# Kernel optimization log

Measured on AMD Instinct MI355X. Metric: run time of the kernel, lower is better.

The kernel has to match this reference:

```python
import jax, jax.numpy as jnp
import numpy as np

B, S, C, H = 2, 3144, 256, 8
HD = C // H                      # head_dim = key_dim = 32
SCALE = HD ** -0.5
QN = 8                           # queriesNum hard-coded in source
KS = 5                           # lepe depthwise conv kernel


def setup_inputs() -> dict:
    key = jax.random.key(0)
    ks = jax.random.split(key, 10)
    gain_qkv = 2 ** (-2.5) * (2.0 / (C + C)) ** 0.5  # xavier_normal std with gain 2^-2.5
    gain_out = (2.0 / (C + C)) ** 0.5
    return {
        "x": jax.random.normal(ks[0], (B, S, C), jnp.float32),
        "mask": jax.random.uniform(ks[1], (B, S, S), jnp.float32),
        "wq": jax.random.normal(ks[2], (C, C), jnp.float32) * gain_qkv,
        "bq": jnp.zeros((C,), jnp.float32),
        "wk": jax.random.normal(ks[3], (C, C), jnp.float32) * gain_qkv,
        "bk": jnp.zeros((C,), jnp.float32),
        "wv": jax.random.normal(ks[4], (C, C), jnp.float32) * gain_qkv,
        "bv": jnp.zeros((C,), jnp.float32),
        "lepe_w": jax.random.normal(ks[5], (KS, KS, 1, C), jnp.float32) * 0.05,  # depthwise HWIO
        "lepe_b": jnp.zeros((C,), jnp.float32),
        "wo": jax.random.normal(ks[6], (C, C), jnp.float32) * gain_out,
        "bo": jnp.zeros((C,), jnp.float32),
        "h": 56,
        "w": 56,
    }


def _dwconv(x_nhwc, kern, bias):
    # depthwise 5x5, stride 1, padding 2 (groups = channels)
    y = jax.lax.conv_general_dilated(
        x_nhwc, kern, window_strides=(1, 1), padding=((2, 2), (2, 2)),
        dimension_numbers=("NHWC", "HWIO", "NHWC"),
        feature_group_count=x_nhwc.shape[-1])
    return y + bias


def reference(x, mask, wq, bq, wk, bk, wv, bv, lepe_w, lepe_b, wo, bo, h, w):
    b, s, c = x.shape
    q = x @ wq.T + bq
    k = (x @ wk.T + bk) * SCALE
    v = x @ wv.T + bv
    # lepe positional residual on the non-query tokens
    lepe = _dwconv(v[:, QN:].reshape(b, h, w, c), lepe_w, lepe_b).reshape(b, h * w, c)
    qh = q.reshape(b, s, H, HD).transpose(0, 2, 1, 3)   # (b, H, s, hd)
    kh = k.reshape(b, s, H, HD).transpose(0, 2, 1, 3)
    vh = kh  # faithful to source: v_h = k.reshape(...)  (scaled k used as values)
    qk = jnp.einsum("bhqd,bhkd->bhqk", qh, kh)
    qk = qk + jnp.log(mask[:, None] + 1e-6)              # isSoftMask=True path
    attn = jax.nn.softmax(qk, axis=-1)
    out = jnp.einsum("bhqk,bhkd->bhqd", attn, vh)
    out = out.transpose(0, 2, 1, 3).reshape(b, s, c)
    out = out.at[:, QN:].add(lepe)
    return out @ wo.T + bo
```

## Files before the change

kernel.cpp:

```cpp
#include <hip/hip_runtime.h>


#define S_LEN 3144
#define SP    3200
#define HEADS 8
#define HD    32
#define BATCH 2
#define MROWS (BATCH*S_LEN)
#define NPIX  3136
#define SCALE_F 0.17677669529663687f
#define KQ_SC   0.25504472665352026f

typedef __bf16 bf16x8  __attribute__((ext_vector_type(8)));
typedef __bf16 bf16x4  __attribute__((ext_vector_type(4)));
typedef float  floatx4 __attribute__((ext_vector_type(4)));
typedef short  shortx4 __attribute__((ext_vector_type(4)));

static __device__ __forceinline__ float bf2f(unsigned int h) {
  union { unsigned int u; float f; } v; v.u = h << 16; return v.f;
}
static __device__ __forceinline__ unsigned short f2bf(float f) {
  union { __bf16 b; unsigned short u; } v; v.b = (__bf16)f; return v.u;
}
static __device__ __forceinline__ bf16x8 ldcvt8(const float* __restrict__ p) {
  float4 a = *(const float4*)p;
  float4 b = *(const float4*)(p + 4);
  bf16x8 r;
  r[0]=(__bf16)a.x; r[1]=(__bf16)a.y; r[2]=(__bf16)a.z; r[3]=(__bf16)a.w;
  r[4]=(__bf16)b.x; r[5]=(__bf16)b.y; r[6]=(__bf16)b.z; r[7]=(__bf16)b.w;
  return r;
}

#define GLOBAL_AS __attribute__((address_space(1)))
#define LDS_AS    __attribute__((address_space(3)))
static __device__ __forceinline__ void gload_lds16(const void* g, void* l) {
  __builtin_amdgcn_global_load_lds((const GLOBAL_AS void*)g, (LDS_AS void*)l, 16, 0, 0);
}

#define FENCE4() asm volatile("s_waitcnt vmcnt(4)" ::: "memory")
#define FENCE0() asm volatile("s_waitcnt vmcnt(0)" ::: "memory")

__global__ __launch_bounds__(256) void k_cvt(
    const float* __restrict__ x, const float* __restrict__ wq,
    const float* __restrict__ wk, const float* __restrict__ wv,
    unsigned short* __restrict__ xb, unsigned short* __restrict__ w3b)
{
  const int i = blockIdx.x * 256 + threadIdx.x;
  const int NX = MROWS * 32;
  const int NW = 8192;
  const float* src;
  unsigned short* dst;
  if (i < NX) { src = x + (size_t)i * 8; dst = xb + (size_t)i * 8; }
  else {
    const int j = i - NX;
    if (j >= 3 * NW) return;
    src = (j < NW) ? wq + (size_t)j * 8
        : (j < 2 * NW) ? wk + (size_t)(j - NW) * 8
                       : wv + (size_t)(j - 2 * NW) * 8;
    dst = w3b + (size_t)j * 8;
  }
  bf16x8 v = ldcvt8(src);
  *(bf16x8*)dst = v;
}

__global__ __launch_bounds__(256) void k_qkv(
    const unsigned short* __restrict__ xb, const unsigned short* __restrict__ w3b,
    const float* __restrict__ bqp, const float* __restrict__ bkp,
    const float* __restrict__ bvp,
    unsigned short* __restrict__ qws, unsigned short* __restrict__ kws,
    unsigned short* __restrict__ vfrag, unsigned short* __restrict__ vstage)
{
  __shared__ unsigned short lds_t[64 * 65];
  const int lane = threadIdx.x & 63;
  const int wid  = threadIdx.x >> 6;
  const int c    = lane & 15, quad = lane >> 4;
  const int bsel  = blockIdx.x / 50;
  const int stile = blockIdx.x % 50;
  const int srow0 = stile * 64;
  const int ncol = blockIdx.y * 64;
  const int wsel = ncol >> 8;
  const int col0 = ncol & 255;

  const float* bptr = (wsel == 0) ? bqp : (wsel == 1) ? bkp : bvp;

  const int srow = srow0 + wid * 16 + c;
  const int arow = bsel * S_LEN + ((srow < S_LEN) ? srow : 0);
  const unsigned short* ap = xb  + (size_t)arow * 256 + quad * 8;
  const unsigned short* bp = w3b + (size_t)(ncol + c) * 256 + quad * 8;

  floatx4 acc[4];
#pragma unroll
  for (int ct = 0; ct < 4; ++ct) acc[ct] = (floatx4){0.f, 0.f, 0.f, 0.f};

#pragma unroll
  for (int ks = 0; ks < 8; ++ks) {
    bf16x8 af = *(const bf16x8*)(ap + ks * 32);
#pragma unroll
    for (int ct = 0; ct < 4; ++ct) {
      bf16x8 bf = *(const bf16x8*)(bp + (size_t)ct * 16 * 256 + ks * 32);
      acc[ct] = __builtin_amdgcn_mfma_f32_16x16x32_bf16(af, bf, acc[ct], 0, 0, 0);
    }
  }

#pragma unroll
  for (int ct = 0; ct < 4; ++ct) {
    const int col = col0 + ct * 16 + c;
    const float bias = bptr[col];
#pragma unroll
    for (int r = 0; r < 4; ++r) {
      const int s = srow0 + wid * 16 + quad * 4 + r;
      const int valid = (s < S_LEN);
      const float v = acc[ct][r] + bias;
      if (wsel == 0) {
        qws[(((size_t)(bsel * HEADS + (col >> 5))) * SP + s) * HD + (col & 31)] =
            valid ? f2bf(v) : (unsigned short)0;
      } else if (wsel == 1) {
        kws[(((size_t)(bsel * HEADS + (col >> 5))) * SP + s) * HD + (col & 31)] =
            valid ? f2bf(v * KQ_SC) : (unsigned short)0;
        lds_t[(ct * 16 + c) * 65 + (wid * 16 + quad * 4 + r)] =
            valid ? f2bf(v * SCALE_F) : (unsigned short)0;
      } else {
        if (valid) vstage[(size_t)(bsel * S_LEN + s) * 256 + col] = f2bf(v);
      }
    }
  }

  if (wsel == 1) {
    __syncthreads();
    const int tid = threadIdx.x;
#pragma unroll
    for (int j = 0; j < 4; ++j) {
      const int grp  = j * 4 + (tid >> 6);
      const int l    = tid & 63;
      const int ct2  = grp & 3;
      const int half = (grp >> 2) & 1;
      const int hsel = grp >> 3;
      const int cc = l & 15, qq = l >> 4;
      const int cl = hsel * 32 + half * 16 + cc;
      const int rb = ct2 * 16 + qq * 4;
      union { shortx4 s4; unsigned short u[4]; } pk;
#pragma unroll
      for (int e = 0; e < 4; ++e) pk.u[e] = lds_t[cl * 65 + rb + e];
      const int hglob = (col0 >> 5) + hsel;
      const size_t off =
          ((((size_t)(bsel * HEADS + hglob) * 50 + stile) * 4 + ct2) * 2 + half) * 64 + l;
      *(shortx4*)(vfrag + off * 4) = pk.s4;
    }
  }
}

__global__ __launch_bounds__(256) void k_lepe(const unsigned short* __restrict__ vws,
                                              const float* __restrict__ cw,
                                              const float* __restrict__ cb,
                                              unsigned short* __restrict__ lepe)
{
  int idx = blockIdx.x * 256 + threadIdx.x;
  if (idx >= BATCH * NPIX * 32) return;
  const int cg = idx & 31;
  const int p  = (idx >> 5) % NPIX;
  const int b  = idx / (NPIX * 32);
  const int y  = p / 56, xx = p - y * 56;

  float acc[8];
  {
    float4 b0 = *(const float4*)(cb + cg * 8);
    float4 b1 = *(const float4*)(cb + cg * 8 + 4);
    acc[0]=b0.x; acc[1]=b0.y; acc[2]=b0.z; acc[3]=b0.w;
    acc[4]=b1.x; acc[5]=b1.y; acc[6]=b1.z; acc[7]=b1.w;
  }
#pragma unroll
  for (int dy = -2; dy <= 2; ++dy) {
    const int yy = y + dy;
    if ((unsigned)yy >= 56u) continue;
#pragma unroll
    for (int dx = -2; dx <= 2; ++dx) {
      const int xs = xx + dx;
      if ((unsigned)xs >= 56u) continue;
      uint4 vv = *(const uint4*)(vws + (size_t)(b * S_LEN + 8 + yy * 56 + xs) * 256 + cg * 8);
      const float* wp = cw + (size_t)((dy + 2) * 5 + (dx + 2)) * 256 + cg * 8;
      float4 w0 = *(const float4*)wp;
      float4 w1 = *(const float4*)(wp + 4);
      unsigned int va[4] = {vv.x, vv.y, vv.z, vv.w};
      acc[0] += bf2f(va[0] & 0xFFFFu) * w0.x;  acc[1] += bf2f(va[0] >> 16) * w0.y;
      acc[2] += bf2f(va[1] & 0xFFFFu) * w0.z;  acc[3] += bf2f(va[1] >> 16) * w0.w;
      acc[4] += bf2f(va[2] & 0xFFFFu) * w1.x;  acc[5] += bf2f(va[2] >> 16) * w1.y;
      acc[6] += bf2f(va[3] & 0xFFFFu) * w1.z;  acc[7] += bf2f(va[3] >> 16) * w1.w;
    }
  }
  unsigned int o[4];
#pragma unroll
  for (int j = 0; j < 4; ++j)
    o[j] = (unsigned int)f2bf(acc[2*j]) | ((unsigned int)f2bf(acc[2*j+1]) << 16);
  *((uint4*)(lepe + (size_t)(b * NPIX + p) * 256 + cg * 8)) = make_uint4(o[0], o[1], o[2], o[3]);
}

template<bool TAIL>
static __device__ __forceinline__ void proc_tile(
    int t, const unsigned short* __restrict__ kb,
    const unsigned short* __restrict__ vb,
    const float* __restrict__ mb,
    int c, int quad, int lane, const bf16x8 qf,
    floatx4& o0, floatx4& o1, float& l_run)
{
  const int k0 = t * 64;
  bf16x8 kf[4]; shortx4 v0[4], v1[4];
  const unsigned short* tb = vb + (size_t)t * 2048;
#pragma unroll
  for (int ct = 0; ct < 4; ++ct) {
    kf[ct] = *(const bf16x8*)(kb + (size_t)(k0 + ct * 16 + c) * HD + quad * 8);
    v0[ct] = *(const shortx4*)(tb + (ct * 2 + 0) * 256 + lane * 4);
    v1[ct] = *(const shortx4*)(tb + (ct * 2 + 1) * 256 + lane * 4);
  }
  floatx4 s[4];
#pragma unroll
  for (int ct = 0; ct < 4; ++ct)
    s[ct] = __builtin_amdgcn_mfma_f32_16x16x32_bf16(kf[ct], qf,
               (floatx4){0.f,0.f,0.f,0.f}, 0, 0, 0);
  float ls = 0.f;
  shortx4 pf[4];
#pragma unroll
  for (int ct = 0; ct < 4; ++ct) {
    const float4 mv = *(const float4*)(mb + c * 64 + (((ct * 4 + quad) ^ c) * 4));
    float pr[4];
    pr[0] = (mv.x + 1e-6f) * __builtin_amdgcn_exp2f(s[ct][0]);
    pr[1] = (mv.y + 1e-6f) * __builtin_amdgcn_exp2f(s[ct][1]);
    pr[2] = (mv.z + 1e-6f) * __builtin_amdgcn_exp2f(s[ct][2]);
    pr[3] = (mv.w + 1e-6f) * __builtin_amdgcn_exp2f(s[ct][3]);
    if (TAIL) {
      const int kk = k0 + ct * 16 + quad * 4;
#pragma unroll
      for (int r = 0; r < 4; ++r) if (kk + r >= S_LEN) pr[r] = 0.f;
    }
    ls += (pr[0] + pr[1]) + (pr[2] + pr[3]);
    union { bf16x4 b4; shortx4 s4; } u;
    u.b4[0]=(__bf16)pr[0]; u.b4[1]=(__bf16)pr[1]; u.b4[2]=(__bf16)pr[2]; u.b4[3]=(__bf16)pr[3];
    pf[ct] = u.s4;
  }
  l_run += ls;
#pragma unroll
  for (int ct = 0; ct < 4; ++ct) {
    o0 = __builtin_amdgcn_mfma_f32_16x16x16bf16_1k(v0[ct], pf[ct], o0, 0, 0, 0);
    o1 = __builtin_amdgcn_mfma_f32_16x16x16bf16_1k(v1[ct], pf[ct], o1, 0, 0, 0);
  }
}

static __device__ __forceinline__ void stage_mask(
    const float* const (&msrc)[4], const int (&goff4)[4], int k0, float* dst)
{
#pragma unroll
  for (int i = 0; i < 4; ++i)
    gload_lds16(msrc[i] + (k0 + goff4[i]), dst + i * 256);
}

static __device__ __forceinline__ void stage_mask_tail(
    const float* const (&msrc)[4], const int (&goff4)[4], int k0, float* dst)
{
#pragma unroll
  for (int i = 0; i < 4; ++i) {
    int kk = k0 + goff4[i];
    if (kk > S_LEN - 4) kk = S_LEN - 4;
    gload_lds16(msrc[i] + kk, dst + i * 256);
  }
}

__global__ __launch_bounds__(512) void k_flash(
    const unsigned short* __restrict__ qws,
    const unsigned short* __restrict__ kws,
    const unsigned short* __restrict__ vfrag,
    const float* __restrict__ mask,
    const unsigned short* __restrict__ lepe,
    unsigned short* __restrict__ attn)
{
  __shared__ __align__(16) float smem[8][2048];
  const int lane = threadIdx.x & 63;
  const int wid  = threadIdx.x >> 6;
  const int c    = lane & 15, quad = lane >> 4;
  const int u    = blockIdx.x;
  const int xcd  = u & 7;
  const int slot = u >> 3;
  const int h    = slot & 7;
  const int p    = (slot >> 3) * 8 + xcd;
  const int b    = p / 200;
  const int strip = p - b * 200;
  const int qrow = strip * 16 + c;
  const size_t bh = (size_t)(b * HEADS + h);

  const bf16x8 qf = *(const bf16x8*)(qws + (bh * SP + qrow) * HD + quad * 8);
  const unsigned short* kb = kws + bh * SP * HD;
  const unsigned short* vb = vfrag + bh * (size_t)(50 * 2048);
  float* mt = &smem[wid][0];

  const float* msrc[4];
  int goff4[4];
#pragma unroll
  for (int i = 0; i < 4; ++i) {
    const int rq = i * 4 + (lane >> 4);
    int mr = strip * 16 + rq; if (mr >= S_LEN) mr = S_LEN - 1;
    msrc[i] = mask + ((size_t)b * S_LEN + mr) * S_LEN;
    goff4[i] = ((lane & 15) ^ rq) * 4;
  }

  float l_run = 0.f;
  floatx4 o0 = (floatx4){0.f,0.f,0.f,0.f};
  floatx4 o1 = (floatx4){0.f,0.f,0.f,0.f};

  const int tbase = wid * 6;
  const int nt = (wid < 2) ? 7 : 6;

  stage_mask(msrc, goff4, tbase * 64, mt);

  for (int it = 0; it < nt; ++it) {
    const int t = (it < 6) ? tbase + it : 48 + wid;
    if (it + 1 < nt) {
      const int tn = (it + 1 < 6) ? tbase + it + 1 : 48 + wid;
      float* dst = mt + ((it + 1) & 1) * 1024;
      if (tn == 49) stage_mask_tail(msrc, goff4, 49 * 64, dst);
      else          stage_mask(msrc, goff4, tn * 64, dst);
      FENCE4();
    } else {
      FENCE0();
    }
    const float* mb = mt + (it & 1) * 1024;
    if (wid == 1 && it == 6)
      proc_tile<true >(t, kb, vb, mb, c, quad, lane, qf, o0, o1, l_run);
    else
      proc_tile<false>(t, kb, vb, mb, c, quad, lane, qf, o0, o1, l_run);
  }

#pragma unroll
  for (int r = 0; r < 4; ++r) {
    smem[wid][lane * 9 + r]     = o0[r];
    smem[wid][lane * 9 + 4 + r] = o1[r];
  }
  smem[wid][lane * 9 + 8] = l_run;
  __syncthreads();

  if (wid == 0) {
#pragma unroll
    for (int w = 1; w < 8; ++w) {
#pragma unroll
      for (int r = 0; r < 4; ++r) {
        o0[r] += smem[w][lane * 9 + r];
        o1[r] += smem[w][lane * 9 + 4 + r];
      }
      l_run += smem[w][lane * 9 + 8];
    }
    l_run += __shfl_xor(l_run, 16);
    l_run += __shfl_xor(l_run, 32);
    const float rl = 1.f / l_run;

    if (qrow < S_LEN) {
      const size_t obase = ((size_t)b * S_LEN + qrow) * 256 + h * 32;
      const size_t lbase = (qrow >= 8) ? (((size_t)b * NPIX + (qrow - 8)) * 256 + h * 32) : 0;
#pragma unroll
      for (int mt2 = 0; mt2 < 2; ++mt2) {
        floatx4 ov = mt2 ? o1 : o0;
#pragma unroll
        for (int r = 0; r < 4; ++r) {
          const int d = mt2 * 16 + quad * 4 + r;
          float val = ov[r] * rl;
          if (qrow >= 8) val += bf2f(lepe[lbase + d]);
          attn[obase + d] = f2bf(val);
        }
      }
    }
  }
}

__global__ __launch_bounds__(256) void k_oproj(
    const unsigned short* __restrict__ attn,
    const float* __restrict__ wop,
    const float* __restrict__ bop,
    float* __restrict__ out)
{
  const int lane = threadIdx.x & 63;
  const int wid  = threadIdx.x >> 6;
  const int c = lane & 15, quad = lane >> 4;
  const int row0 = blockIdx.x * 64 + wid * 16;
  const int col0 = blockIdx.y * 64;

  int arow = row0 + c; if (arow >= MROWS) arow = 0;
  const unsigned short* ap = attn + (size_t)arow * 256 + quad * 8;
  const float* bp = wop + (size_t)(col0 + c) * 256 + quad * 8;

  floatx4 acc[4];
#pragma unroll
  for (int ct = 0; ct < 4; ++ct) acc[ct] = (floatx4){0.f,0.f,0.f,0.f};
#pragma unroll
  for (int ks = 0; ks < 8; ++ks) {
    bf16x8 af = *(const bf16x8*)(ap + ks * 32);
#pragma unroll
    for (int ct = 0; ct < 4; ++ct) {
      bf16x8 bf = ldcvt8(bp + (size_t)ct * 16 * 256 + ks * 32);
      acc[ct] = __builtin_amdgcn_mfma_f32_16x16x32_bf16(af, bf, acc[ct], 0, 0, 0);
    }
  }
#pragma unroll
  for (int ct = 0; ct < 4; ++ct) {
    const int col = col0 + ct * 16 + c;
    const float bias = bop[col];
#pragma unroll
    for (int r = 0; r < 4; ++r) {
      const int row = row0 + quad * 4 + r;
      if (row >= MROWS) continue;
      out[(size_t)row * 256 + col] = acc[ct][r] + bias;
    }
  }
}

#define QW_OFF 0u
#define KW_OFF 3276800u
#define VF_OFF 6553600u
#define LE_OFF 9830400u
#define AT_OFF 13041664u

extern "C" void kernel_launch(void* const* d_in, const int* in_sizes, int n_in,
                              void* d_out, int out_size, void* d_ws, size_t ws_size,
                              hipStream_t stream) {
  const float* x    = (const float*)d_in[0];
  const float* mask = (const float*)d_in[1];
  const float* wq   = (const float*)d_in[2];
  const float* bq   = (const float*)d_in[3];
  const float* wk   = (const float*)d_in[4];
  const float* bk   = (const float*)d_in[5];
  const float* wv   = (const float*)d_in[6];
  const float* bv   = (const float*)d_in[7];
  const float* lw   = (const float*)d_in[8];
  const float* lb   = (const float*)d_in[9];
  const float* wo   = (const float*)d_in[10];
  const float* bo   = (const float*)d_in[11];

  char* ws = (char*)d_ws;
  unsigned short* qws = (unsigned short*)(ws + QW_OFF);
  unsigned short* kws = (unsigned short*)(ws + KW_OFF);
  unsigned short* vfr = (unsigned short*)(ws + VF_OFF);
  unsigned short* w3b = (unsigned short*)(ws + LE_OFF);
  unsigned short* lpe = (unsigned short*)(ws + LE_OFF);
  unsigned short* atb = (unsigned short*)(ws + AT_OFF);
  unsigned short* vst = (unsigned short*)d_out;
  unsigned short* xb  = (unsigned short*)d_out + 1609728;
  float*          outf = (float*)d_out;

  k_cvt<<<882, 256, 0, stream>>>(x, wq, wk, wv, xb, w3b);
  k_qkv<<<dim3(100, 12), 256, 0, stream>>>(xb, w3b, bq, bk, bv, qws, kws, vfr, vst);
  k_lepe<<<784, 256, 0, stream>>>(vst, lw, lb, lpe);
  k_flash<<<3200, 512, 0, stream>>>(qws, kws, vfr, mask, lpe, atb);
  k_oproj<<<dim3(99, 4), 256, 0, stream>>>(atb, wo, bo, outf);
}
```

Before: 311.8 us.

## Prefetch K/V register fragments one tile ahead alongside mask staging

The attention loop is split into a load phase and a compute phase. K and V fragments for the next 64-key tile are now issued into a second register set at the same time as the async mask staging, and the loop is unrolled in pairs to alternate between the two buffers. The wait is raised to vmcnt(16) so the next tile's 16 loads can stay in flight while the current tile computes. This is meant to hide global-load latency on K/V, at the cost of more VGPRs, which could lower occupancy.

```diff
diff --git a/kernel.cpp b/kernel.cpp
--- a/kernel.cpp
+++ b/kernel.cpp
@@ -37,8 +37,8 @@
   __builtin_amdgcn_global_load_lds((const GLOBAL_AS void*)g, (LDS_AS void*)l, 16, 0, 0);
 }
 
-#define FENCE4() asm volatile("s_waitcnt vmcnt(4)" ::: "memory")
-#define FENCE0() asm volatile("s_waitcnt vmcnt(0)" ::: "memory")
+#define FENCE16() asm volatile("s_waitcnt vmcnt(16)" ::: "memory")
+#define FENCE0()  asm volatile("s_waitcnt vmcnt(0)" ::: "memory")
 
 __global__ __launch_bounds__(256) void k_cvt(
     const float* __restrict__ x, const float* __restrict__ wq,
@@ -194,16 +194,12 @@
   *((uint4*)(lepe + (size_t)(b * NPIX + p) * 256 + cg * 8)) = make_uint4(o[0], o[1], o[2], o[3]);
 }
 
-template<bool TAIL>
-static __device__ __forceinline__ void proc_tile(
-    int t, const unsigned short* __restrict__ kb,
-    const unsigned short* __restrict__ vb,
-    const float* __restrict__ mb,
-    int c, int quad, int lane, const bf16x8 qf,
-    floatx4& o0, floatx4& o1, float& l_run)
+static __device__ __forceinline__ void kv_load(
+    const unsigned short* __restrict__ kb, const unsigned short* __restrict__ vb,
+    int t, int c, int quad, int lane,
+    bf16x8 (&kf)[4], shortx4 (&v0)[4], shortx4 (&v1)[4])
 {
   const int k0 = t * 64;
-  bf16x8 kf[4]; shortx4 v0[4], v1[4];
   const unsigned short* tb = vb + (size_t)t * 2048;
 #pragma unroll
   for (int ct = 0; ct < 4; ++ct) {
@@ -211,6 +207,14 @@
     v0[ct] = *(const shortx4*)(tb + (ct * 2 + 0) * 256 + lane * 4);
     v1[ct] = *(const shortx4*)(tb + (ct * 2 + 1) * 256 + lane * 4);
   }
+}
+
+template<bool TAIL>
+static __device__ __forceinline__ void tile_compute(
+    int k0, const bf16x8 (&kf)[4], const shortx4 (&v0)[4], const shortx4 (&v1)[4],
+    const float* __restrict__ mb, int c, int quad, const bf16x8 qf,
+    floatx4& o0, floatx4& o1, float& l_run)
+{
   floatx4 s[4];
 #pragma unroll
   for (int ct = 0; ct < 4; ++ct)
@@ -305,26 +309,41 @@
   floatx4 o1 = (floatx4){0.f,0.f,0.f,0.f};
 
   const int tbase = wid * 6;
-  const int nt = (wid < 2) ? 7 : 6;
+  const bool hasExtra = (wid < 2);
+
+  bf16x8 kfA[4], kfB[4];
+  shortx4 v0A[4], v1A[4], v0B[4], v1B[4];
 
   stage_mask(msrc, goff4, tbase * 64, mt);
-
-  for (int it = 0; it < nt; ++it) {
-    const int t = (it < 6) ? tbase + it : 48 + wid;
-    if (it + 1 < nt) {
-      const int tn = (it + 1 < 6) ? tbase + it + 1 : 48 + wid;
-      float* dst = mt + ((it + 1) & 1) * 1024;
-      if (tn == 49) stage_mask_tail(msrc, goff4, 49 * 64, dst);
-      else          stage_mask(msrc, goff4, tn * 64, dst);
-      FENCE4();
+  kv_load(kb, vb, tbase, c, quad, lane, kfA, v0A, v1A);
+
+#pragma unroll 1
+  for (int jp = 0; jp < 3; ++jp) {
+    const int j0 = 2 * jp;
+    stage_mask(msrc, goff4, (tbase + j0 + 1) * 64, mt + 1024);
+    kv_load(kb, vb, tbase + j0 + 1, c, quad, lane, kfB, v0B, v1B);
+    FENCE16();
+    tile_compute<false>(0, kfA, v0A, v1A, mt, c, quad, qf, o0, o1, l_run);
+    if (jp < 2) {
+      stage_mask(msrc, goff4, (tbase + j0 + 2) * 64, mt);
+      kv_load(kb, vb, tbase + j0 + 2, c, quad, lane, kfA, v0A, v1A);
+      FENCE16();
+    } else if (hasExtra) {
+      if (wid == 0) stage_mask(msrc, goff4, 48 * 64, mt);
+      else          stage_mask_tail(msrc, goff4, 49 * 64, mt);
+      kv_load(kb, vb, 48 + wid, c, quad, lane, kfA, v0A, v1A);
+      FENCE16();
     } else {
       FENCE0();
     }
-    const float* mb = mt + (it & 1) * 1024;
-    if (wid == 1 && it == 6)
-      proc_tile<true >(t, kb, vb, mb, c, quad, lane, qf, o0, o1, l_run);
+    tile_compute<false>(0, kfB, v0B, v1B, mt + 1024, c, quad, qf, o0, o1, l_run);
+  }
+  if (hasExtra) {
+    FENCE0();
+    if (wid == 0)
+      tile_compute<false>(48 * 64, kfA, v0A, v1A, mt, c, quad, qf, o0, o1, l_run);
     else
-      proc_tile<false>(t, kb, vb, mb, c, quad, lane, qf, o0, o1, l_run);
+      tile_compute<true >(49 * 64, kfA, v0A, v1A, mt, c, quad, qf, o0, o1, l_run);
   }
 
 #pragma unroll
```

After: 345.9 us. +10.9%, slower.

## Put all eight heads in one flash block, split keys in halves, read mask directly

Applied to the files above, without the earlier changes.

The flash kernel now runs 400 blocks of 1024 threads. Each block covers one 16-row query strip for all 8 heads, and each head's key range is split across two waves. The old design staged the mask into LDS through global_load_lds double buffering. Now each lane reads its mask row straight from global memory, so the 8 head-waves sharing a strip can reuse the same mask rows through cache instead of fetching them 8 times across different blocks. The trade-offs are fewer, larger blocks (lower occupancy granularity), uncoalesced per-lane float4 mask reads, and longer serial loops per wave with no explicit prefetch.

```diff
diff --git a/kernel.cpp b/kernel.cpp
--- a/kernel.cpp
+++ b/kernel.cpp
@@ -30,15 +30,6 @@
   r[4]=(__bf16)b.x; r[5]=(__bf16)b.y; r[6]=(__bf16)b.z; r[7]=(__bf16)b.w;
   return r;
 }
-
-#define GLOBAL_AS __attribute__((address_space(1)))
-#define LDS_AS    __attribute__((address_space(3)))
-static __device__ __forceinline__ void gload_lds16(const void* g, void* l) {
-  __builtin_amdgcn_global_load_lds((const GLOBAL_AS void*)g, (LDS_AS void*)l, 16, 0, 0);
-}
-
-#define FENCE4() asm volatile("s_waitcnt vmcnt(4)" ::: "memory")
-#define FENCE0() asm volatile("s_waitcnt vmcnt(0)" ::: "memory")
 
 __global__ __launch_bounds__(256) void k_cvt(
     const float* __restrict__ x, const float* __restrict__ wq,
@@ -198,7 +189,7 @@
 static __device__ __forceinline__ void proc_tile(
     int t, const unsigned short* __restrict__ kb,
     const unsigned short* __restrict__ vb,
-    const float* __restrict__ mb,
+    const float* __restrict__ mp,
     int c, int quad, int lane, const bf16x8 qf,
     floatx4& o0, floatx4& o1, float& l_run)
 {
@@ -220,14 +211,16 @@
   shortx4 pf[4];
 #pragma unroll
   for (int ct = 0; ct < 4; ++ct) {
-    const float4 mv = *(const float4*)(mb + c * 64 + (((ct * 4 + quad) ^ c) * 4));
+    int kk = k0 + ct * 16 + quad * 4;
+    int kkl = kk;
+    if (TAIL) { if (kkl > S_LEN - 4) kkl = S_LEN - 4; }
+    const float4 mv = *(const float4*)(mp + kkl);
     float pr[4];
     pr[0] = (mv.x + 1e-6f) * __builtin_amdgcn_exp2f(s[ct][0]);
     pr[1] = (mv.y + 1e-6f) * __builtin_amdgcn_exp2f(s[ct][1]);
     pr[2] = (mv.z + 1e-6f) * __builtin_amdgcn_exp2f(s[ct][2]);
     pr[3] = (mv.w + 1e-6f) * __builtin_amdgcn_exp2f(s[ct][3]);
     if (TAIL) {
-      const int kk = k0 + ct * 16 + quad * 4;
 #pragma unroll
       for (int r = 0; r < 4; ++r) if (kk + r >= S_LEN) pr[r] = 0.f;
     }
@@ -244,26 +237,7 @@
   }
 }
 
-static __device__ __forceinline__ void stage_mask(
-    const float* const (&msrc)[4], const int (&goff4)[4], int k0, float* dst)
-{
-#pragma unroll
-  for (int i = 0; i < 4; ++i)
-    gload_lds16(msrc[i] + (k0 + goff4[i]), dst + i * 256);
-}
-
-static __device__ __forceinline__ void stage_mask_tail(
-    const float* const (&msrc)[4], const int (&goff4)[4], int k0, float* dst)
-{
-#pragma unroll
-  for (int i = 0; i < 4; ++i) {
-    int kk = k0 + goff4[i];
-    if (kk > S_LEN - 4) kk = S_LEN - 4;
-    gload_lds16(msrc[i] + kk, dst + i * 256);
-  }
-}
-
-__global__ __launch_bounds__(512) void k_flash(
+__global__ __launch_bounds__(1024) void k_flash(
     const unsigned short* __restrict__ qws,
     const unsigned short* __restrict__ kws,
     const unsigned short* __restrict__ vfrag,
@@ -271,80 +245,57 @@
     const unsigned short* __restrict__ lepe,
     unsigned short* __restrict__ attn)
 {
-  __shared__ __align__(16) float smem[8][2048];
+  __shared__ __align__(16) float red[8][64][9];
   const int lane = threadIdx.x & 63;
   const int wid  = threadIdx.x >> 6;
+  const int h    = wid & 7;
+  const int khalf = wid >> 3;
   const int c    = lane & 15, quad = lane >> 4;
+
   const int u    = blockIdx.x;
   const int xcd  = u & 7;
-  const int slot = u >> 3;
-  const int h    = slot & 7;
-  const int p    = (slot >> 3) * 8 + xcd;
-  const int b    = p / 200;
-  const int strip = p - b * 200;
+  const int j    = u >> 3;
+  const int b    = xcd & 1;
+  const int strip = j * 4 + (xcd >> 1);
   const int qrow = strip * 16 + c;
   const size_t bh = (size_t)(b * HEADS + h);
 
   const bf16x8 qf = *(const bf16x8*)(qws + (bh * SP + qrow) * HD + quad * 8);
   const unsigned short* kb = kws + bh * SP * HD;
   const unsigned short* vb = vfrag + bh * (size_t)(50 * 2048);
-  float* mt = &smem[wid][0];
-
-  const float* msrc[4];
-  int goff4[4];
-#pragma unroll
-  for (int i = 0; i < 4; ++i) {
-    const int rq = i * 4 + (lane >> 4);
-    int mr = strip * 16 + rq; if (mr >= S_LEN) mr = S_LEN - 1;
-    msrc[i] = mask + ((size_t)b * S_LEN + mr) * S_LEN;
-    goff4[i] = ((lane & 15) ^ rq) * 4;
-  }
+  const int mrow = (qrow < S_LEN) ? qrow : (S_LEN - 1);
+  const float* mp = mask + ((size_t)b * S_LEN + mrow) * S_LEN;
 
   float l_run = 0.f;
   floatx4 o0 = (floatx4){0.f,0.f,0.f,0.f};
   floatx4 o1 = (floatx4){0.f,0.f,0.f,0.f};
 
-  const int tbase = wid * 6;
-  const int nt = (wid < 2) ? 7 : 6;
-
-  stage_mask(msrc, goff4, tbase * 64, mt);
-
-  for (int it = 0; it < nt; ++it) {
-    const int t = (it < 6) ? tbase + it : 48 + wid;
-    if (it + 1 < nt) {
-      const int tn = (it + 1 < 6) ? tbase + it + 1 : 48 + wid;
-      float* dst = mt + ((it + 1) & 1) * 1024;
-      if (tn == 49) stage_mask_tail(msrc, goff4, 49 * 64, dst);
-      else          stage_mask(msrc, goff4, tn * 64, dst);
-      FENCE4();
-    } else {
-      FENCE0();
-    }
-    const float* mb = mt + (it & 1) * 1024;
-    if (wid == 1 && it == 6)
-      proc_tile<true >(t, kb, vb, mb, c, quad, lane, qf, o0, o1, l_run);
-    else
-      proc_tile<false>(t, kb, vb, mb, c, quad, lane, qf, o0, o1, l_run);
-  }
-
-#pragma unroll
-  for (int r = 0; r < 4; ++r) {
-    smem[wid][lane * 9 + r]     = o0[r];
-    smem[wid][lane * 9 + 4 + r] = o1[r];
-  }
-  smem[wid][lane * 9 + 8] = l_run;
+  const int t0 = khalf * 25;
+#pragma unroll 1
+  for (int jt = 0; jt < 24; ++jt)
+    proc_tile<false>(t0 + jt, kb, vb, mp, c, quad, lane, qf, o0, o1, l_run);
+  if (khalf == 0)
+    proc_tile<false>(24, kb, vb, mp, c, quad, lane, qf, o0, o1, l_run);
+  else
+    proc_tile<true >(49, kb, vb, mp, c, quad, lane, qf, o0, o1, l_run);
+
+  if (khalf) {
+#pragma unroll
+    for (int r = 0; r < 4; ++r) {
+      red[h][lane][r]     = o0[r];
+      red[h][lane][4 + r] = o1[r];
+    }
+    red[h][lane][8] = l_run;
+  }
   __syncthreads();
 
-  if (wid == 0) {
-#pragma unroll
-    for (int w = 1; w < 8; ++w) {
-#pragma unroll
-      for (int r = 0; r < 4; ++r) {
-        o0[r] += smem[w][lane * 9 + r];
-        o1[r] += smem[w][lane * 9 + 4 + r];
-      }
-      l_run += smem[w][lane * 9 + 8];
-    }
+  if (!khalf) {
+#pragma unroll
+    for (int r = 0; r < 4; ++r) {
+      o0[r] += red[h][lane][r];
+      o1[r] += red[h][lane][4 + r];
+    }
+    l_run += red[h][lane][8];
     l_run += __shfl_xor(l_run, 16);
     l_run += __shfl_xor(l_run, 32);
     const float rl = 1.f / l_run;
@@ -444,6 +395,6 @@
   k_cvt<<<882, 256, 0, stream>>>(x, wq, wk, wv, xb, w3b);
   k_qkv<<<dim3(100, 12), 256, 0, stream>>>(xb, w3b, bq, bk, bv, qws, kws, vfr, vst);
   k_lepe<<<784, 256, 0, stream>>>(vst, lw, lb, lpe);
-  k_flash<<<3200, 512, 0, stream>>>(qws, kws, vfr, mask, lpe, atb);
+  k_flash<<<400, 1024, 0, stream>>>(qws, kws, vfr, mask, lpe, atb);
   k_oproj<<<dim3(99, 4), 256, 0, stream>>>(atb, wo, bo, outf);
 }
```

New measurement: 337.7 us. +8.3%, slower.

## Precompute log2 mask into tiled swizzled layout before flash attention

Applied to the files above, without the earlier changes.

Adds a k_mprep kernel that converts the soft mask to log2(mask+1e-6) and writes it into a per-strip, per-tile swizzled buffer, with -1e30 in the padded tail columns. The flash kernel then streams this buffer contiguously and folds the mask into the exponent as exp2(s + logm), which removes the per-element multiply, the tail-masking branch and the clamped tail loads. The old path is kept as a fallback for when the workspace is too small for the roughly 82 MB buffer. The price is an extra full pass over the mask: one read plus one write of a slightly larger buffer. That traffic is likely to outweigh what the flash kernel saves.

```diff
diff --git a/kernel.cpp b/kernel.cpp
--- a/kernel.cpp
+++ b/kernel.cpp
@@ -61,6 +61,36 @@
   }
   bf16x8 v = ldcvt8(src);
   *(bf16x8*)dst = v;
+}
+
+__global__ __launch_bounds__(256) void k_mprep(const float* __restrict__ mask,
+                                               float* __restrict__ pm)
+{
+  const int bs = blockIdx.x;
+  const int b  = bs / 200, strip = bs % 200;
+  const int tid = threadIdx.x;
+  const int i  = tid >> 6, l = tid & 63;
+  const int rq = i * 4 + (l >> 4);
+  int mr = strip * 16 + rq; if (mr >= S_LEN) mr = S_LEN - 1;
+  const int cg = ((l & 15) ^ rq) & 15;
+  const float* src = mask + ((size_t)b * S_LEN + mr) * S_LEN;
+  float* dst = pm + (size_t)bs * (50 * 1024) + tid * 4;
+#pragma unroll 1
+  for (int tt = 0; tt < 10; ++tt) {
+    const int t = blockIdx.y * 10 + tt;
+    const int c0 = t * 64 + cg * 4;
+    float4 o;
+    if (c0 < S_LEN) {
+      float4 mv = *(const float4*)(src + c0);
+      o.x = __log2f(mv.x + 1e-6f);
+      o.y = __log2f(mv.y + 1e-6f);
+      o.z = __log2f(mv.z + 1e-6f);
+      o.w = __log2f(mv.w + 1e-6f);
+    } else {
+      o = make_float4(-1e30f, -1e30f, -1e30f, -1e30f);
+    }
+    *(float4*)(dst + (size_t)t * 1024) = o;
+  }
 }
 
 __global__ __launch_bounds__(256) void k_qkv(
@@ -194,8 +224,7 @@
   *((uint4*)(lepe + (size_t)(b * NPIX + p) * 256 + cg * 8)) = make_uint4(o[0], o[1], o[2], o[3]);
 }
 
-template<bool TAIL>
-static __device__ __forceinline__ void proc_tile(
+static __device__ __forceinline__ void proc_tile_pre(
     int t, const unsigned short* __restrict__ kb,
     const unsigned short* __restrict__ vb,
     const float* __restrict__ mb,
@@ -222,15 +251,10 @@
   for (int ct = 0; ct < 4; ++ct) {
     const float4 mv = *(const float4*)(mb + c * 64 + (((ct * 4 + quad) ^ c) * 4));
     float pr[4];
-    pr[0] = (mv.x + 1e-6f) * __builtin_amdgcn_exp2f(s[ct][0]);
-    pr[1] = (mv.y + 1e-6f) * __builtin_amdgcn_exp2f(s[ct][1]);
-    pr[2] = (mv.z + 1e-6f) * __builtin_amdgcn_exp2f(s[ct][2]);
-    pr[3] = (mv.w + 1e-6f) * __builtin_amdgcn_exp2f(s[ct][3]);
-    if (TAIL) {
-      const int kk = k0 + ct * 16 + quad * 4;
-#pragma unroll
-      for (int r = 0; r < 4; ++r) if (kk + r >= S_LEN) pr[r] = 0.f;
-    }
+    pr[0] = __builtin_amdgcn_exp2f(s[ct][0] + mv.x);
+    pr[1] = __builtin_amdgcn_exp2f(s[ct][1] + mv.y);
+    pr[2] = __builtin_amdgcn_exp2f(s[ct][2] + mv.z);
+    pr[3] = __builtin_amdgcn_exp2f(s[ct][3] + mv.w);
     ls += (pr[0] + pr[1]) + (pr[2] + pr[3]);
     union { bf16x4 b4; shortx4 s4; } u;
     u.b4[0]=(__bf16)pr[0]; u.b4[1]=(__bf16)pr[1]; u.b4[2]=(__bf16)pr[2]; u.b4[3]=(__bf16)pr[3];
@@ -244,30 +268,19 @@
   }
 }
 
-static __device__ __forceinline__ void stage_mask(
-    const float* const (&msrc)[4], const int (&goff4)[4], int k0, float* dst)
+static __device__ __forceinline__ void stage_pre(
+    const float* __restrict__ mp_t, int lane, float* dst)
 {
 #pragma unroll
   for (int i = 0; i < 4; ++i)
-    gload_lds16(msrc[i] + (k0 + goff4[i]), dst + i * 256);
-}
-
-static __device__ __forceinline__ void stage_mask_tail(
-    const float* const (&msrc)[4], const int (&goff4)[4], int k0, float* dst)
-{
-#pragma unroll
-  for (int i = 0; i < 4; ++i) {
-    int kk = k0 + goff4[i];
-    if (kk > S_LEN - 4) kk = S_LEN - 4;
-    gload_lds16(msrc[i] + kk, dst + i * 256);
-  }
-}
-
-__global__ __launch_bounds__(512) void k_flash(
+    gload_lds16(mp_t + i * 256 + lane * 4, dst + i * 256);
+}
+
+__global__ __launch_bounds__(512) void k_flash_pre(
     const unsigned short* __restrict__ qws,
     const unsigned short* __restrict__ kws,
     const unsigned short* __restrict__ vfrag,
-    const float* __restrict__ mask,
+    const float* __restrict__ pmask,
     const unsigned short* __restrict__ lepe,
     unsigned short* __restrict__ attn)
 {
@@ -288,17 +301,8 @@
   const bf16x8 qf = *(const bf16x8*)(qws + (bh * SP + qrow) * HD + quad * 8);
   const unsigned short* kb = kws + bh * SP * HD;
   const unsigned short* vb = vfrag + bh * (size_t)(50 * 2048);
+  const float* mpb = pmask + (size_t)(b * 200 + strip) * (50 * 1024);
   float* mt = &smem[wid][0];
-
-  const float* msrc[4];
-  int goff4[4];
-#pragma unroll
-  for (int i = 0; i < 4; ++i) {
-    const int rq = i * 4 + (lane >> 4);
-    int mr = strip * 16 + rq; if (mr >= S_LEN) mr = S_LEN - 1;
-    msrc[i] = mask + ((size_t)b * S_LEN + mr) * S_LEN;
-    goff4[i] = ((lane & 15) ^ rq) * 4;
-  }
 
   float l_run = 0.f;
   floatx4 o0 = (floatx4){0.f,0.f,0.f,0.f};
@@ -307,24 +311,18 @@
   const int tbase = wid * 6;
   const int nt = (wid < 2) ? 7 : 6;
 
-  stage_mask(msrc, goff4, tbase * 64, mt);
+  stage_pre(mpb + tbase * 1024, lane, mt);
 
   for (int it = 0; it < nt; ++it) {
     const int t = (it < 6) ? tbase + it : 48 + wid;
     if (it + 1 < nt) {
       const int tn = (it + 1 < 6) ? tbase + it + 1 : 48 + wid;
-      float* dst = mt + ((it + 1) & 1) * 1024;
-      if (tn == 49) stage_mask_tail(msrc, goff4, 49 * 64, dst);
-      else          stage_mask(msrc, goff4, tn * 64, dst);
+      stage_pre(mpb + tn * 1024, lane, mt + ((it + 1) & 1) * 1024);
       FENCE4();
     } else {
       FENCE0();
     }
-    const float* mb = mt + (it & 1) * 1024;
-    if (wid == 1 && it == 6)
-      proc_tile<true >(t, kb, vb, mb, c, quad, lane, qf, o0, o1, l_run);
-    else
-      proc_tile<false>(t, kb, vb, mb, c, quad, lane, qf, o0, o1, l_run);
+    proc_tile_pre(t, kb, vb, mt + (it & 1) * 1024, c, quad, lane, qf, o0, o1, l_run);
   }
 
 #pragma unroll
@@ -367,6 +365,179 @@
   }
 }
 
+template<bool TAIL>
+static __device__ __forceinline__ void proc_tile_fb(
+    int t, const unsigned short* __restrict__ kb,
+    const unsigned short* __restrict__ vb,
+    const float* __restrict__ mb,
+    int c, int quad, int lane, const bf16x8 qf,
+    floatx4& o0, floatx4& o1, float& l_run)
+{
+  const int k0 = t * 64;
+  bf16x8 kf[4]; shortx4 v0[4], v1[4];
+  const unsigned short* tb = vb + (size_t)t * 2048;
+#pragma unroll
+  for (int ct = 0; ct < 4; ++ct) {
+    kf[ct] = *(const bf16x8*)(kb + (size_t)(k0 + ct * 16 + c) * HD + quad * 8);
+    v0[ct] = *(const shortx4*)(tb + (ct * 2 + 0) * 256 + lane * 4);
+    v1[ct] = *(const shortx4*)(tb + (ct * 2 + 1) * 256 + lane * 4);
+  }
+  floatx4 s[4];
+#pragma unroll
+  for (int ct = 0; ct < 4; ++ct)
+    s[ct] = __builtin_amdgcn_mfma_f32_16x16x32_bf16(kf[ct], qf,
+               (floatx4){0.f,0.f,0.f,0.f}, 0, 0, 0);
+  float ls = 0.f;
+  shortx4 pf[4];
+#pragma unroll
+  for (int ct = 0; ct < 4; ++ct) {
+    const float4 mv = *(const float4*)(mb + c * 64 + (((ct * 4 + quad) ^ c) * 4));
+    float pr[4];
+    pr[0] = (mv.x + 1e-6f) * __builtin_amdgcn_exp2f(s[ct][0]);
+    pr[1] = (mv.y + 1e-6f) * __builtin_amdgcn_exp2f(s[ct][1]);
+    pr[2] = (mv.z + 1e-6f) * __builtin_amdgcn_exp2f(s[ct][2]);
+    pr[3] = (mv.w + 1e-6f) * __builtin_amdgcn_exp2f(s[ct][3]);
+    if (TAIL) {
+      const int kk = k0 + ct * 16 + quad * 4;
+#pragma unroll
+      for (int r = 0; r < 4; ++r) if (kk + r >= S_LEN) pr[r] = 0.f;
+    }
+    ls += (pr[0] + pr[1]) + (pr[2] + pr[3]);
+    union { bf16x4 b4; shortx4 s4; } u;
+    u.b4[0]=(__bf16)pr[0]; u.b4[1]=(__bf16)pr[1]; u.b4[2]=(__bf16)pr[2]; u.b4[3]=(__bf16)pr[3];
+    pf[ct] = u.s4;
+  }
+  l_run += ls;
+#pragma unroll
+  for (int ct = 0; ct < 4; ++ct) {
+    o0 = __builtin_amdgcn_mfma_f32_16x16x16bf16_1k(v0[ct], pf[ct], o0, 0, 0, 0);
+    o1 = __builtin_amdgcn_mfma_f32_16x16x16bf16_1k(v1[ct], pf[ct], o1, 0, 0, 0);
+  }
+}
+
+static __device__ __forceinline__ void stage_mask_fb(
+    const float* const (&msrc)[4], const int (&goff4)[4], int k0, float* dst)
+{
+#pragma unroll
+  for (int i = 0; i < 4; ++i)
+    gload_lds16(msrc[i] + (k0 + goff4[i]), dst + i * 256);
+}
+
+static __device__ __forceinline__ void stage_mask_tail_fb(
+    const float* const (&msrc)[4], const int (&goff4)[4], int k0, float* dst)
+{
+#pragma unroll
+  for (int i = 0; i < 4; ++i) {
+    int kk = k0 + goff4[i];
+    if (kk > S_LEN - 4) kk = S_LEN - 4;
+    gload_lds16(msrc[i] + kk, dst + i * 256);
+  }
+}
+
+__global__ __launch_bounds__(512) void k_flash_fb(
+    const unsigned short* __restrict__ qws,
+    const unsigned short* __restrict__ kws,
+    const unsigned short* __restrict__ vfrag,
+    const float* __restrict__ mask,
+    const unsigned short* __restrict__ lepe,
+    unsigned short* __restrict__ attn)
+{
+  __shared__ __align__(16) float smem[8][2048];
+  const int lane = threadIdx.x & 63;
+  const int wid  = threadIdx.x >> 6;
+  const int c    = lane & 15, quad = lane >> 4;
+  const int u    = blockIdx.x;
+  const int xcd  = u & 7;
+  const int slot = u >> 3;
+  const int h    = slot & 7;
+  const int p    = (slot >> 3) * 8 + xcd;
+  const int b    = p / 200;
+  const int strip = p - b * 200;
+  const int qrow = strip * 16 + c;
+  const size_t bh = (size_t)(b * HEADS + h);
+
+  const bf16x8 qf = *(const bf16x8*)(qws + (bh * SP + qrow) * HD + quad * 8);
+  const unsigned short* kb = kws + bh * SP * HD;
+  const unsigned short* vb = vfrag + bh * (size_t)(50 * 2048);
+  float* mt = &smem[wid][0];
+
+  const float* msrc[4];
+  int goff4[4];
+#pragma unroll
+  for (int i = 0; i < 4; ++i) {
+    const int rq = i * 4 + (lane >> 4);
+    int mr = strip * 16 + rq; if (mr >= S_LEN) mr = S_LEN - 1;
+    msrc[i] = mask + ((size_t)b * S_LEN + mr) * S_LEN;
+    goff4[i] = ((lane & 15) ^ rq) * 4;
+  }
+
+  float l_run = 0.f;
+  floatx4 o0 = (floatx4){0.f,0.f,0.f,0.f};
+  floatx4 o1 = (floatx4){0.f,0.f,0.f,0.f};
+
+  const int tbase = wid * 6;
+  const int nt = (wid < 2) ? 7 : 6;
+
+  stage_mask_fb(msrc, goff4, tbase * 64, mt);
+
+  for (int it = 0; it < nt; ++it) {
+    const int t = (it < 6) ? tbase + it : 48 + wid;
+    if (it + 1 < nt) {
+      const int tn = (it + 1 < 6) ? tbase + it + 1 : 48 + wid;
+      float* dst = mt + ((it + 1) & 1) * 1024;
+      if (tn == 49) stage_mask_tail_fb(msrc, goff4, 49 * 64, dst);
+      else          stage_mask_fb(msrc, goff4, tn * 64, dst);
+      FENCE4();
+    } else {
+      FENCE0();
+    }
+    const float* mb = mt + (it & 1) * 1024;
+    if (wid == 1 && it == 6)
+      proc_tile_fb<true >(t, kb, vb, mb, c, quad, lane, qf, o0, o1, l_run);
+    else
+      proc_tile_fb<false>(t, kb, vb, mb, c, quad, lane, qf, o0, o1, l_run);
+  }
+
+#pragma unroll
+  for (int r = 0; r < 4; ++r) {
+    smem[wid][lane * 9 + r]     = o0[r];
+    smem[wid][lane * 9 + 4 + r] = o1[r];
+  }
+  smem[wid][lane * 9 + 8] = l_run;
+  __syncthreads();
+
+  if (wid == 0) {
+#pragma unroll
+    for (int w = 1; w < 8; ++w) {
+#pragma unroll
+      for (int r = 0; r < 4; ++r) {
+        o0[r] += smem[w][lane * 9 + r];
+        o1[r] += smem[w][lane * 9 + 4 + r];
+      }
+      l_run += smem[w][lane * 9 + 8];
+    }
+    l_run += __shfl_xor(l_run, 16);
+    l_run += __shfl_xor(l_run, 32);
+    const float rl = 1.f / l_run;
+
+    if (qrow < S_LEN) {
+      const size_t obase = ((size_t)b * S_LEN + qrow) * 256 + h * 32;
+      const size_t lbase = (qrow >= 8) ? (((size_t)b * NPIX + (qrow - 8)) * 256 + h * 32) : 0;
+#pragma unroll
+      for (int mt2 = 0; mt2 < 2; ++mt2) {
+        floatx4 ov = mt2 ? o1 : o0;
+#pragma unroll
+        for (int r = 0; r < 4; ++r) {
+          const int d = mt2 * 16 + quad * 4 + r;
+          float val = ov[r] * rl;
+          if (qrow >= 8) val += bf2f(lepe[lbase + d]);
+          attn[obase + d] = f2bf(val);
+        }
+      }
+    }
+  }
+}
+
 __global__ __launch_bounds__(256) void k_oproj(
     const unsigned short* __restrict__ attn,
     const float* __restrict__ wop,
@@ -413,6 +584,8 @@
 #define VF_OFF 6553600u
 #define LE_OFF 9830400u
 #define AT_OFF 13041664u
+#define PM_OFF 16261120u
+#define PM_NEED (16261120u + 81920000u)
 
 extern "C" void kernel_launch(void* const* d_in, const int* in_sizes, int n_in,
                               void* d_out, int out_size, void* d_ws, size_t ws_size,
@@ -441,9 +614,19 @@
   unsigned short* xb  = (unsigned short*)d_out + 1609728;
   float*          outf = (float*)d_out;
 
+  const bool use_pre = (ws_size >= (size_t)PM_NEED);
+
   k_cvt<<<882, 256, 0, stream>>>(x, wq, wk, wv, xb, w3b);
-  k_qkv<<<dim3(100, 12), 256, 0, stream>>>(xb, w3b, bq, bk, bv, qws, kws, vfr, vst);
-  k_lepe<<<784, 256, 0, stream>>>(vst, lw, lb, lpe);
-  k_flash<<<3200, 512, 0, stream>>>(qws, kws, vfr, mask, lpe, atb);
+  if (use_pre) {
+    float* pm = (float*)(ws + PM_OFF);
+    k_mprep<<<dim3(400, 5), 256, 0, stream>>>(mask, pm);
+    k_qkv<<<dim3(100, 12), 256, 0, stream>>>(xb, w3b, bq, bk, bv, qws, kws, vfr, vst);
+    k_lepe<<<784, 256, 0, stream>>>(vst, lw, lb, lpe);
+    k_flash_pre<<<3200, 512, 0, stream>>>(qws, kws, vfr, pm, lpe, atb);
+  } else {
+    k_qkv<<<dim3(100, 12), 256, 0, stream>>>(xb, w3b, bq, bk, bv, qws, kws, vfr, vst);
+    k_lepe<<<784, 256, 0, stream>>>(vst, lw, lb, lpe);
+    k_flash_fb<<<3200, 512, 0, stream>>>(qws, kws, vfr, mask, lpe, atb);
+  }
   k_oproj<<<dim3(99, 4), 256, 0, stream>>>(atb, wo, bo, outf);
 }
```

New measurement: 326.7 us. 1.05x slower.
